# Performance work log

Measured on AMD Instinct MI355X. Metric: run time of the kernel, lower is better.

Reference implementation:

```python
import jax, jax.numpy as jnp
import numpy as np

# Module config (matches init_kwargs)
K_W, K_H = 3, 3
C_IN, C_OUT = 64, 64
B, W_IN, H_IN = 8, 32, 32
J = K_W * K_H * C_IN  # flattened patch length, torch layout (c_in, k_w, k_h)


def setup_inputs() -> dict:
    key = jax.random.key(0)
    k_x, k_w = jax.random.split(key)
    x = jax.random.normal(k_x, (B, W_IN, H_IN, C_IN), dtype=jnp.float32)
    # reset_parameters: randint{0,1} * 2 - 1 -> weights in {-1, +1}
    weights = jax.random.randint(k_w, (C_OUT, J), 0, 2).astype(jnp.float32) * 2.0 - 1.0
    return {"input": x, "weights": weights}


def reference(input, weights):
    b, w_in, h_in, c_in = input.shape
    pw, ph = K_W // 2, K_H // 2
    # F.pad(..., value=-1) pads the two spatial dims, channels untouched
    xp = jnp.pad(input, ((0, 0), (pw, pw), (ph, ph), (0, 0)), constant_values=-1.0)
    # torch .unfold(1,k_w,1).unfold(2,k_h,1) -> (B, W, H, c_in, k_w, k_h)
    patches = jnp.stack(
        [jnp.stack([xp[:, u:u + w_in, v:v + h_in, :] for v in range(K_H)], axis=-1)
         for u in range(K_W)],
        axis=-2,
    )  # (B, W, H, c_in, k_w, k_h)
    # flatten patch, then view flat axis as (k_w, k_h*c_in) exactly like the
    # torch reshape([-1, k_w, k_h*c_in]) (a pure regrouping of the flat axis)
    u = patches.reshape(b * w_in * h_in, K_W, K_H * c_in)  # (N, k_w, k_h*c_in)
    wv = weights.reshape(C_OUT, K_W, K_H * c_in)            # (A, k_w, k_h*c_in)
    # einsum('bj,aj->baj') then sum over the k_w-sized chunk axis == contract u
    inter = jnp.einsum('nug,aug->nag', u, wv)               # (N, c_out, k_h*c_in)
    # majority vote: clamp to [-1,1], scale by 3, reduce
    out = jnp.sum(jnp.clip(inter, -1.0, 1.0) * 3.0, axis=-1)  # (N, c_out)
    return out.reshape(b, w_in, h_in, C_OUT)
```

## Files before the change

kernel.cpp:

```cpp
#include <hip/hip_runtime.h>


typedef unsigned int u32;
typedef float f4 __attribute__((ext_vector_type(4)));
typedef _Float16 h8 __attribute__((ext_vector_type(8)));
typedef __fp16 hp2 __attribute__((ext_vector_type(2)));
typedef u32 uu2 __attribute__((ext_vector_type(2)));
typedef int i4 __attribute__((ext_vector_type(4)));

#define HS    19
#define PLANE (64 * HS)
#define NP    16

__device__ __forceinline__ float clip1(float s) {
    return __builtin_amdgcn_fmed3f(s, -1.0f, 1.0f);
}

__device__ __forceinline__ int ybi(int G, int p) {
    return ((G >> 1) * NP + p) * 4 + (G & 1) * 2;
}

__global__ __launch_bounds__(192) void prep_kernel(const float* __restrict__ w,
                                                   u32* __restrict__ M32) {
    const int a = blockIdx.x, G = threadIdx.x;
    const float w1 = w[a * 576 + G];
    const float w2 = w[a * 576 + 192 + G];
    const float w3 = w[a * 576 + 384 + G];
    const int q = ((w1 * w2 < 0.f) ? 2 : 0) + ((w1 * w3 < 0.f) ? 1 : 0);
    const u32 s1 = (w1 < 0.f) ? 0xBC00u : 0x3C00u;
    const u32 v0 = (q == 0) ? s1 : 0u, v1 = (q == 1) ? s1 : 0u;
    const u32 v2 = (q == 2) ? s1 : 0u, v3 = (q == 3) ? s1 : 0u;
    M32[a * 384 + G * 2 + 0] = v0 | (v1 << 16);
    M32[a * 384 + G * 2 + 1] = v2 | (v3 << 16);
}

template <int R0>
__device__ __forceinline__ void phaseA_12(const float* __restrict__ xt,
                                          u32* __restrict__ yb,
                                          int ci0, int p) {
#pragma unroll
    for (int d = 0; d < 12; ++d) {
        const int r    = (R0 + d) % 9;
        const int cinc = (R0 + d) / 9;
        const int uv1 = r;           const int cA = 0;
        const int uv2 = (r + 3) % 9; const int cB = 21 + (r + 3) / 9;
        const int uv3 = (r + 6) % 9; const int cC = 42 + (r + 6) / 9;
        const int ci = ci0 + cinc;
        const float x1 = xt[(uv1 / 3) * PLANE + (ci + cA) * HS + p + (uv1 % 3)];
        const float x2 = xt[(uv2 / 3) * PLANE + (ci + cB) * HS + p + (uv2 % 3)];
        const float x3 = xt[(uv3 / 3) * PLANE + (ci + cC) * HS + p + (uv3 % 3)];
        const float sp = x1 + x2, sm = x1 - x2;
        const float y0 = clip1(sp + x3), y1 = clip1(sp - x3);
        const float y2 = clip1(sm + x3), y3 = clip1(sm - x3);
        hp2 lo = __builtin_amdgcn_cvt_pkrtz(y0, y1);
        hp2 hi = __builtin_amdgcn_cvt_pkrtz(y2, y3);
        uu2 pr;
        pr.x = __builtin_bit_cast(u32, lo);
        pr.y = __builtin_bit_cast(u32, hi);
        const int G = 9 * ci + r;
        *(uu2*)&yb[ybi(G, p)] = pr;
    }
}

__global__ __launch_bounds__(256, 2) void maj3_kernel(
        const float* __restrict__ x, const u32* __restrict__ M32,
        float* __restrict__ out) {
    __shared__ float xt[3 * PLANE];
    __shared__ u32  yb[96 * NP * 4];

    const int tid   = threadIdx.x;
    const int lane  = tid & 63;
    const int wid   = tid >> 6;
    const int blk   = blockIdx.x;
    const int hhalf = blk & 1;
    const int bw    = blk >> 1;
    const int bimg  = bw >> 5, wrow = bw & 31;
    const int h0    = hhalf * NP;

    const int p16 = lane & 15, sub = lane >> 4;
    const int a0  = wid * 16;

    const int c = lane;
    const float* xb = x + (bimg * 32 * 32) * 64 + c;
    float vs[14];
#pragma unroll
    for (int j = 0; j < 14; ++j) {
        const int i = wid + 4 * j;
        const int u = i / 18, hh = i - u * 18;
        const int wx = wrow - 1 + u, hx = h0 - 1 + hh;
        float v = -1.0f;
        if (i < 54 && (unsigned)wx < 32u && (unsigned)hx < 32u)
            v = xb[(wx * 32 + hx) * 64];
        vs[j] = v;
    }

    const u32* mp = M32 + (a0 + p16) * 384 + sub * 4;
    i4 af[24];
#pragma unroll
    for (int st = 0; st < 24; ++st)
        af[st] = *(const i4*)(mp + st * 16);

#pragma unroll
    for (int j = 0; j < 14; ++j) {
        const int i = wid + 4 * j;
        if (i < 54) {
            const int u = i / 18, hh = i - u * 18;
            xt[u * PLANE + c * HS + hh] = vs[j];
        }
    }
    __syncthreads();

    {
        const int s = wid * 4 + sub;
        const int ci0 = (4 * s) / 3;
        const int sel = s % 3;
        if (sel == 0)      phaseA_12<0>(xt, yb, ci0, p16);
        else if (sel == 1) phaseA_12<3>(xt, yb, ci0, p16);
        else               phaseA_12<6>(xt, yb, ci0, p16);
    }
    __syncthreads();

    {
        f4 acc = {0.f, 0.f, 0.f, 0.f};
#pragma unroll
        for (int st = 0; st < 24; ++st) {
            i4 bi = *(const i4*)&yb[((st * 4 + sub) * NP + p16) * 4];
            acc = __builtin_amdgcn_mfma_f32_16x16x32_f16(
                      __builtin_bit_cast(h8, af[st]),
                      __builtin_bit_cast(h8, bi), acc, 0, 0, 0);
        }

        const int n = bw * 32 + h0 + p16;
        float* op = out + n * 64 + a0 + sub * 4;
        f4 o;
#pragma unroll
        for (int r = 0; r < 4; ++r) o[r] = 3.0f * acc[r];
        *(f4*)op = o;
    }
}

extern "C" void kernel_launch(void* const* d_in, const int* in_sizes, int n_in,
                              void* d_out, int out_size, void* d_ws, size_t ws_size,
                              hipStream_t stream) {
    const float* x = (const float*)d_in[0];
    const float* w = (const float*)d_in[1];
    float* out = (float*)d_out;
    u32* M32 = (u32*)d_ws;
    prep_kernel<<<64, 192, 0, stream>>>(w, M32);
    maj3_kernel<<<512, 256, 0, stream>>>(x, M32, out);
}
```

Measured before the change: 66.17 us.

## Fuse weight-prep into main kernel and pipeline weight-fragment building with MFMA

Removes the separate prep_kernel launch and has each thread build its fp16 selector weight fragments directly from the raw float weights. Weight loads are split into three chunks so the next chunk's global loads overlap the current chunk's MFMA loop. This removes one kernel launch and the workspace round trip. In exchange every block redoes the sign/quadrant conversion, adding ALU work and register pressure (two 24-element float2 staging arrays).

```diff
diff --git a/kernel.cpp b/kernel.cpp
--- a/kernel.cpp
+++ b/kernel.cpp
@@ -3,6 +3,7 @@
 
 typedef unsigned int u32;
 typedef float f4 __attribute__((ext_vector_type(4)));
+typedef float f2v __attribute__((ext_vector_type(2)));
 typedef _Float16 h8 __attribute__((ext_vector_type(8)));
 typedef __fp16 hp2 __attribute__((ext_vector_type(2)));
 typedef u32 uu2 __attribute__((ext_vector_type(2)));
@@ -20,18 +21,36 @@
     return ((G >> 1) * NP + p) * 4 + (G & 1) * 2;
 }
 
-__global__ __launch_bounds__(192) void prep_kernel(const float* __restrict__ w,
-                                                   u32* __restrict__ M32) {
-    const int a = blockIdx.x, G = threadIdx.x;
-    const float w1 = w[a * 576 + G];
-    const float w2 = w[a * 576 + 192 + G];
-    const float w3 = w[a * 576 + 384 + G];
-    const int q = ((w1 * w2 < 0.f) ? 2 : 0) + ((w1 * w3 < 0.f) ? 1 : 0);
+__device__ __forceinline__ void mk_float(float w1, float w2, float w3,
+                                         u32& lo, u32& hi) {
+    const int q  = ((w1 * w2 < 0.f) ? 2 : 0) + ((w1 * w3 < 0.f) ? 1 : 0);
     const u32 s1 = (w1 < 0.f) ? 0xBC00u : 0x3C00u;
     const u32 v0 = (q == 0) ? s1 : 0u, v1 = (q == 1) ? s1 : 0u;
     const u32 v2 = (q == 2) ? s1 : 0u, v3 = (q == 3) ? s1 : 0u;
-    M32[a * 384 + G * 2 + 0] = v0 | (v1 << 16);
-    M32[a * 384 + G * 2 + 1] = v2 | (v3 << 16);
+    lo = v0 | (v1 << 16);
+    hi = v2 | (v3 << 16);
+}
+
+__device__ __forceinline__ void load_chunk(const float* __restrict__ wb,
+                                           int g, f2v wch[8][3]) {
+#pragma unroll
+    for (int t = 0; t < 8; ++t) {
+        const int st = g * 8 + t;
+        wch[t][0] = *(const f2v*)(wb + st * 8);
+        wch[t][1] = *(const f2v*)(wb + st * 8 + 192);
+        wch[t][2] = *(const f2v*)(wb + st * 8 + 384);
+    }
+}
+
+__device__ __forceinline__ void build_chunk(const f2v wch[8][3], i4 afg[8]) {
+#pragma unroll
+    for (int t = 0; t < 8; ++t) {
+        u32 lo0, hi0, lo1, hi1;
+        mk_float(wch[t][0].x, wch[t][1].x, wch[t][2].x, lo0, hi0);
+        mk_float(wch[t][0].y, wch[t][1].y, wch[t][2].y, lo1, hi1);
+        i4 v; v.x = (int)lo0; v.y = (int)hi0; v.z = (int)lo1; v.w = (int)hi1;
+        afg[t] = v;
+    }
 }
 
 template <int R0>
@@ -63,7 +82,7 @@
 }
 
 __global__ __launch_bounds__(256, 2) void maj3_kernel(
-        const float* __restrict__ x, const u32* __restrict__ M32,
+        const float* __restrict__ x, const float* __restrict__ w,
         float* __restrict__ out) {
     __shared__ float xt[3 * PLANE];
     __shared__ u32  yb[96 * NP * 4];
@@ -94,12 +113,6 @@
         vs[j] = v;
     }
 
-    const u32* mp = M32 + (a0 + p16) * 384 + sub * 4;
-    i4 af[24];
-#pragma unroll
-    for (int st = 0; st < 24; ++st)
-        af[st] = *(const i4*)(mp + st * 16);
-
 #pragma unroll
     for (int j = 0; j < 14; ++j) {
         const int i = wid + 4 * j;
@@ -108,6 +121,10 @@
             xt[u * PLANE + c * HS + hh] = vs[j];
         }
     }
+
+    const float* wb = w + (a0 + p16) * 576 + sub * 2;
+    f2v wA[8][3];
+    load_chunk(wb, 0, wA);
     __syncthreads();
 
     {
@@ -122,11 +139,38 @@
 
     {
         f4 acc = {0.f, 0.f, 0.f, 0.f};
+        f2v wBc[8][3], wCc[8][3];
+        i4 afg[8];
+
+        load_chunk(wb, 1, wBc);
+        build_chunk(wA, afg);
 #pragma unroll
-        for (int st = 0; st < 24; ++st) {
-            i4 bi = *(const i4*)&yb[((st * 4 + sub) * NP + p16) * 4];
+        for (int t = 0; t < 8; ++t) {
+            const int st = t;
+            const i4 bi = *(const i4*)&yb[((st * 4 + sub) * NP + p16) * 4];
             acc = __builtin_amdgcn_mfma_f32_16x16x32_f16(
-                      __builtin_bit_cast(h8, af[st]),
+                      __builtin_bit_cast(h8, afg[t]),
+                      __builtin_bit_cast(h8, bi), acc, 0, 0, 0);
+        }
+
+        load_chunk(wb, 2, wCc);
+        build_chunk(wBc, afg);
+#pragma unroll
+        for (int t = 0; t < 8; ++t) {
+            const int st = 8 + t;
+            const i4 bi = *(const i4*)&yb[((st * 4 + sub) * NP + p16) * 4];
+            acc = __builtin_amdgcn_mfma_f32_16x16x32_f16(
+                      __builtin_bit_cast(h8, afg[t]),
+                      __builtin_bit_cast(h8, bi), acc, 0, 0, 0);
+        }
+
+        build_chunk(wCc, afg);
+#pragma unroll
+        for (int t = 0; t < 8; ++t) {
+            const int st = 16 + t;
+            const i4 bi = *(const i4*)&yb[((st * 4 + sub) * NP + p16) * 4];
+            acc = __builtin_amdgcn_mfma_f32_16x16x32_f16(
+                      __builtin_bit_cast(h8, afg[t]),
                       __builtin_bit_cast(h8, bi), acc, 0, 0, 0);
         }
 
@@ -145,7 +189,6 @@
     const float* x = (const float*)d_in[0];
     const float* w = (const float*)d_in[1];
     float* out = (float*)d_out;
-    u32* M32 = (u32*)d_ws;
-    prep_kernel<<<64, 192, 0, stream>>>(w, M32);
-    maj3_kernel<<<512, 256, 0, stream>>>(x, M32, out);
+    (void)d_ws; (void)ws_size;
+    maj3_kernel<<<512, 256, 0, stream>>>(x, w, out);
 }
```

Result: slower. 73.11 us (+10.5%).
